# Optimization experiments

Hardware: AMD Instinct MI355X
Metric: run time of the kernel (lower is better)

Reference implementation:

```python
import jax, jax.numpy as jnp
import numpy as np

B, C, L = 32, 64, 4096
LEVEL, FL, DIM, HID = 3, 8, 64, 64
MID = max(1, C // 4)
REG = 0.01
ODE_STEPS, ODE_H = 10, 0.1  # fixed-step integration of t in [0,1] (eval_t final point)


def _gelu(x):
    return jax.nn.gelu(x, approximate=False)  # torch nn.GELU default is exact erf


def _conv1d(x, w, b, pad, mode):
    # x: [B,Cin,L], w: [Cout,Cin,K] -> [B,Cout,L] (cross-correlation, like torch)
    if pad:
        x = jnp.pad(x, ((0, 0), (0, 0), (pad, pad)), mode=mode)
    y = jax.lax.conv_general_dilated(x, w, (1,), 'VALID',
                                     dimension_numbers=('NCH', 'OIH', 'NCH'))
    return y + b[None, :, None]


def _conv1x1(x, w, b):
    return jnp.einsum('oc,bcl->bol', w, x) + b[None, :, None]


def setup_inputs() -> dict:
    key = jax.random.key(0)
    ks = jax.random.split(key, 12)
    rn = lambda k, s: jax.random.normal(k, s, jnp.float32) * 0.05
    return {
        'x': jax.random.normal(ks[0], (B, C, L), jnp.float32),
        'ode_c1_w': rn(ks[1], (DIM, C, 3)),
        'ode_c1_b': jnp.zeros((DIM,), jnp.float32),
        'ode_c2_w': rn(ks[2], (C, DIM, 3)),
        'ode_c2_b': jnp.zeros((C,), jnp.float32),
        'damp': jnp.float32(0.01),
        'stat_w': rn(ks[3], (HID, C)),
        'stat_b': jnp.zeros((HID,), jnp.float32),
        'gen1_w': rn(ks[4], (2 * HID, HID)),
        'gen1_b': jnp.zeros((2 * HID,), jnp.float32),
        'gen2_w': rn(ks[5], (2 * FL, 2 * HID)),
        'gen2_b': jnp.zeros((2 * FL,), jnp.float32),
        'gate_w': rn(ks[6], (LEVEL, C, C, 3)),
        'gate_b': jnp.zeros((LEVEL, C), jnp.float32),
        'att_w1': rn(ks[7], (LEVEL - 1, MID, C)),
        'att_b1': jnp.zeros((LEVEL - 1, MID), jnp.float32),
        'att_w2': rn(ks[8], (LEVEL - 1, C, MID)),
        'att_b2': jnp.zeros((LEVEL - 1, C), jnp.float32),
    }


def _forward(x, ode_c1_w, ode_c1_b, ode_c2_w, ode_c2_b, damp,
             stat_w, stat_b, gen1_w, gen1_b, gen2_w, gen2_b,
             gate_w, gate_b, att_w1, att_b1, att_w2, att_b2):
    # --- WaveletODE_Pro: autonomous vector field, fixed-step RK4 over [0,1] ---
    def f(z):
        h = _gelu(_conv1d(z, ode_c1_w, ode_c1_b, 1, 'edge'))
        h = jnp.tanh(_conv1d(h, ode_c2_w, ode_c2_b, 1, 'edge'))
        return h - damp * z

    def rk4(z, _):
        k1 = f(z)
        k2 = f(z + 0.5 * ODE_H * k1)
        k3 = f(z + 0.5 * ODE_H * k2)
        k4 = f(z + ODE_H * k3)
        return z + (ODE_H / 6.0) * (k1 + 2 * k2 + 2 * k3 + k4), None

    x_evolved, _ = jax.lax.scan(rk4, x, None, length=ODE_STEPS)

    # --- DyWAN_Pro: per-sample wavelet filter generation + regularizers ---
    def dywan(a):
        stat = _gelu(a.mean(-1) @ stat_w.T + stat_b)               # [B,HID]
        g = _gelu(stat @ gen1_w.T + gen1_b) @ gen2_w.T + gen2_b     # [B,2F]
        lo, hi = g[:, :FL], g[:, FL:]
        lo_pad = jnp.pad(lo, ((0, 0), (1, 1)))                      # zero pad=1, kernel [-1,1]
        lo_smooth = jnp.abs(lo_pad[:, 1:] - lo_pad[:, :-1]).mean()
        lo_n = lo / (jnp.linalg.norm(lo, axis=1, keepdims=True) + 1e-8)
        shift = sum(jnp.abs(lo_n[:, :, None] * jnp.roll(lo_n, s, axis=1)[:, None, :]).mean()
                    for s in range(1, 4))
        amp = jnp.abs((lo_n ** 2).sum(1) - 1.0).mean()
        return lo, hi, REG * (shift + amp) + 0.1 * lo_smooth

    pad_l, pad_r = FL // 2, FL - FL // 2 - 1
    approx = x_evolved
    details, los, his = [], [], []
    ortho = jnp.float32(0.0)
    for _ in range(LEVEL):
        lo, hi, o = dywan(approx)
        ortho = ortho + o
        los.append(lo)
        his.append(hi)
        ap = jnp.pad(approx, ((0, 0), (0, 0), (pad_l, pad_r)), mode='edge')
        # per-sample filter shared across channels: grouped conv == windowed einsum
        win = jnp.stack([ap[:, :, k:k + L] for k in range(FL)], axis=-1)  # [B,C,L,F]
        new_approx = jnp.einsum('bclk,bk->bcl', win, lo)
        details.append(jnp.einsum('bclk,bk->bcl', win, hi))
        approx = new_approx

    # --- CrossScaleFusion: yl input is the INITIAL evolved approx (coeffs[0]) ---
    cur = x_evolved
    enhanced = []
    for i in range(LEVEL - 1, -1, -1):
        det = details[i]
        if i < LEVEL - 1:
            att = jax.nn.sigmoid(_conv1x1(_gelu(_conv1x1(cur, att_w1[i], att_b1[i])),
                                          att_w2[i], att_b2[i]))
            det = det * att + det
        gate = jax.nn.sigmoid(_conv1d(cur, gate_w[i], gate_b[i], 1, 'constant'))
        cur = cur + gate * det
        enhanced.append(det)
    enhanced.reverse()
    return (cur, enhanced[0], enhanced[1], enhanced[2], ortho,
            jnp.stack(los), jnp.stack(his))


def reference(x, ode_c1_w, ode_c1_b, ode_c2_w, ode_c2_b, damp,
              stat_w, stat_b, gen1_w, gen1_b, gen2_w, gen2_b,
              gate_w, gate_b, att_w1, att_b1, att_w2, att_b2):
    return _forward(x, ode_c1_w, ode_c1_b, ode_c2_w, ode_c2_b, damp,
                    stat_w, stat_b, gen1_w, gen1_b, gen2_w, gen2_b,
                    gate_w, gate_b, att_w1, att_b1, att_w2, att_b2)
```

## Files before the change

kernel.cpp:

```cpp
#include <hip/hip_runtime.h>

#define Bn   32
#define Cn   64
#define Ln   4096
#define Nn   (Bn*Cn*Ln)
#define FLn  8
#define MIDn 16
#define TILE3 64
#define NT   64

typedef __bf16 bf16_t;
typedef bf16_t bf16x4 __attribute__((ext_vector_type(4)));
typedef bf16_t bf16x8 __attribute__((ext_vector_type(8)));
typedef float  f32x4  __attribute__((ext_vector_type(4)));

__device__ __forceinline__ float tanh_fast(float x) {
    float ax = fabsf(x);
    float t  = __expf(-2.0f * ax);
    float r  = __fmaf_rn(-2.0f, __fdividef(t, 1.0f + t), 1.0f);
    return copysignf(r, x);
}
__device__ __forceinline__ float gelu_fast(float x) {
    float x3 = x * x * x;
    float u  = 0.7978845608028654f * __fmaf_rn(0.044715f, x3, x);
    return 0.5f * x * (1.0f + tanh_fast(u));
}
__device__ __forceinline__ float sigmoid_f(float x) {
    return 1.0f / (1.0f + __expf(-x));
}

__global__ __launch_bounds__(256) void prep_weights(
    const float* __restrict__ w1, const float* __restrict__ w2,
    const float* __restrict__ gw, const float* __restrict__ aw2,
    bf16_t* __restrict__ w1f, bf16_t* __restrict__ w2f,
    float* __restrict__ gwt, float* __restrict__ aw2t)
{
    int idx = blockIdx.x*256 + threadIdx.x;
    if (idx < 1536) {
        int lane = idx & 63;
        int f  = (idx >> 6) % 6;
        int mt = (idx >> 6) / 6;
        int tau = f >> 1, kc = f & 1;
        int oc = mt*16 + (lane & 15);
        int c0 = kc*32 + (lane >> 4)*8;
        #pragma unroll
        for (int e = 0; e < 8; ++e) {
            int c = c0 + e;
            w1f[idx*8 + e] = (bf16_t)w1[oc*192 + c*3 + tau];
            w2f[idx*8 + e] = (bf16_t)w2[oc*192 + c*3 + tau];
        }
    }
    if (idx < 3*64*192) {
        int lvl = idx / 12288, rem = idx % 12288;
        int oc = rem / 192, r = rem % 192;
        gwt[lvl*12288 + r*64 + oc] = gw[idx];
    }
    if (idx < 2*64*16) {
        int lvl = idx / 1024, rem = idx % 1024;
        int oc = rem / 16, mm = rem % 16;
        aw2t[lvl*1024 + mm*64 + oc] = aw2[idx];
    }
}

__global__ __launch_bounds__(256, 2) void ode_rk4_step(
    const float* __restrict__ zsrc, float* __restrict__ zdst,
    const bf16_t* __restrict__ w1f, const float* __restrict__ b1,
    const bf16_t* __restrict__ w2f, const float* __restrict__ b2,
    const float* __restrict__ damp_p)
{
    __shared__ bf16_t ZC[80*64];
    __shared__ bf16_t HT[80*64];
    __shared__ bf16_t Z0[80*64];
    __shared__ bf16_t SUMB[64*64];

    const int tid  = threadIdx.x;
    const int w    = tid >> 6;
    const int lane = tid & 63;
    const int c15  = lane & 15;
    const int hb   = lane >> 4;
    const int oc0  = w*16 + hb*4;
    const int b    = blockIdx.y;
    const int l0   = blockIdx.x * NT;
    const size_t bbase = (size_t)b * Cn * Ln;
    const float damp = damp_p[0];
    const int pmin = (blockIdx.x == 0) ? 8 : 0;
    const int pmax = (blockIdx.x == gridDim.x - 1) ? 71 : 79;

    #pragma unroll
    for (int jj = 0; jj < 4; ++jj) {
        const int cc0 = (w << 4) + jj*4;
        const float* zr0 = zsrc + bbase + (size_t)(cc0+0) * Ln;
        const float* zr1 = zsrc + bbase + (size_t)(cc0+1) * Ln;
        const float* zr2 = zsrc + bbase + (size_t)(cc0+2) * Ln;
        const float* zr3 = zsrc + bbase + (size_t)(cc0+3) * Ln;
        #pragma unroll
        for (int m2 = 0; m2 < 2; ++m2) {
            int p = lane + (m2 << 6);
            if (p < 80) {
                int l = l0 - 8 + p;
                l = l < 0 ? 0 : (l > Ln-1 ? Ln-1 : l);
                bf16x4 v;
                v[0] = (bf16_t)zr0[l]; v[1] = (bf16_t)zr1[l];
                v[2] = (bf16_t)zr2[l]; v[3] = (bf16_t)zr3[l];
                int off = p*64 + (cc0 ^ ((p & 7) << 3));
                *(bf16x4*)&ZC[off] = v;
                *(bf16x4*)&Z0[off] = v;
            }
        }
    }

    f32x4 bias1v, bias2v;
    #pragma unroll
    for (int j = 0; j < 4; ++j) {
        bias1v[j] = b1[oc0 + j];
        bias2v[j] = b2[oc0 + j];
    }
    bf16x8 af1[6], af2[6];
    {
        const bf16x8* wp1 = (const bf16x8*)w1f + (w*6)*64 + lane;
        const bf16x8* wp2 = (const bf16x8*)w2f + (w*6)*64 + lane;
        #pragma unroll
        for (int f = 0; f < 6; ++f) { af1[f] = wp1[f*64]; af2[f] = wp2[f*64]; }
    }

    __syncthreads();

    for (int i = 0; i < 4; ++i) {
        const int hLo = 2*i + 1, hHi = 79 - 2*i;
        const int kLo = 2*i + 2, kHi = 78 - 2*i;

        #pragma unroll
        for (int nt = 0; nt < 5; ++nt) {
            int ph = nt*16 + c15;
            f32x4 acc = bias1v;
            #pragma unroll
            for (int tau = 0; tau < 3; ++tau) {
                int p = ph + tau - 1;
                p = p < pmin ? pmin : (p > pmax ? pmax : p);
                int base = p*64 + ((hb*8) ^ ((p & 7) << 3));
                acc = __builtin_amdgcn_mfma_f32_16x16x32_bf16(
                    af1[tau*2+0], *(const bf16x8*)&ZC[base], acc, 0, 0, 0);
                acc = __builtin_amdgcn_mfma_f32_16x16x32_bf16(
                    af1[tau*2+1], *(const bf16x8*)&ZC[base ^ 32], acc, 0, 0, 0);
            }
            if (ph >= hLo && ph < hHi) {
                bf16x4 hv;
                #pragma unroll
                for (int j = 0; j < 4; ++j)
                    hv[j] = (bf16_t)gelu_fast(acc[j]);
                *(bf16x4*)&HT[ph*64 + (oc0 ^ ((ph & 7) << 3))] = hv;
            }
        }
        __syncthreads();

        #pragma unroll
        for (int nt = 0; nt < 5; ++nt) {
            int pk = nt*16 + c15;
            f32x4 acc = bias2v;
            #pragma unroll
            for (int tau = 0; tau < 3; ++tau) {
                int q = pk + tau - 1;
                q = q < pmin ? pmin : (q > pmax ? pmax : q);
                int base = q*64 + ((hb*8) ^ ((q & 7) << 3));
                acc = __builtin_amdgcn_mfma_f32_16x16x32_bf16(
                    af2[tau*2+0], *(const bf16x8*)&HT[base], acc, 0, 0, 0);
                acc = __builtin_amdgcn_mfma_f32_16x16x32_bf16(
                    af2[tau*2+1], *(const bf16x8*)&HT[base ^ 32], acc, 0, 0, 0);
            }
            const int col = oc0 ^ ((pk & 7) << 3);
            const int off = pk*64 + col;
            if (i < 3) {
                if (pk >= kLo && pk < kHi) {
                    bf16x4 zc = *(const bf16x4*)&ZC[off];
                    bf16x4 z0 = *(const bf16x4*)&Z0[off];
                    const float alpha = (i == 2) ? 0.10f : 0.05f;
                    const bool inS = (pk >= 8) && (pk < 72);
                    const int soff = (pk-8)*64 + col;
                    bf16x4 sv;
                    if (i > 0 && inS) sv = *(const bf16x4*)&SUMB[soff];
                    bf16x4 wv, nsv;
                    #pragma unroll
                    for (int j = 0; j < 4; ++j) {
                        float kv = tanh_fast(acc[j]) - damp * (float)zc[j];
                        wv[j]  = (bf16_t)((float)z0[j] + alpha * kv);
                        nsv[j] = (i == 0) ? (bf16_t)kv
                                          : (bf16_t)((float)sv[j] + 2.0f * kv);
                    }
                    *(bf16x4*)&ZC[off] = wv;
                    if (inS) *(bf16x4*)&SUMB[soff] = nsv;
                }
            } else {
                if (pk >= 8 && pk < 72) {
                    bf16x4 zc = *(const bf16x4*)&ZC[off];
                    bf16x4 sv = *(const bf16x4*)&SUMB[(pk-8)*64 + col];
                    int gcol = l0 + pk - 8;
                    #pragma unroll
                    for (int j = 0; j < 4; ++j) {
                        float kv = tanh_fast(acc[j]) - damp * (float)zc[j];
                        size_t gof = bbase + (size_t)(oc0 + j)*Ln + gcol;
                        zdst[gof] = zsrc[gof] + (0.1f/6.0f) * ((float)sv[j] + kv);
                    }
                }
            }
        }
        if (i < 3) __syncthreads();
    }
}

__global__ __launch_bounds__(256) void mean_kernel(const float* __restrict__ in, float* __restrict__ m)
{
    const int bc = blockIdx.x;
    const float* __restrict__ row = in + (size_t)bc*Ln;
    float s = 0.0f;
    for (int l = threadIdx.x; l < Ln; l += 256) s += row[l];
    #pragma unroll
    for (int off = 32; off > 0; off >>= 1) s += __shfl_down(s, off, 64);
    __shared__ float red[4];
    if ((threadIdx.x & 63) == 0) red[threadIdx.x >> 6] = s;
    __syncthreads();
    if (threadIdx.x == 0) m[bc] = (red[0]+red[1]+red[2]+red[3]) * (1.0f/Ln);
}

__global__ __launch_bounds__(256) void dywan_kernel(
    const float* __restrict__ m,
    const float* __restrict__ stat_w, const float* __restrict__ stat_b,
    const float* __restrict__ gen1_w, const float* __restrict__ gen1_b,
    const float* __restrict__ gen2_w, const float* __restrict__ gen2_b,
    float* __restrict__ tail, int lvl)
{
    __shared__ float m_s[Bn][Cn];
    __shared__ float stat_s[Bn][64];
    __shared__ float g1_s[Bn][128];
    __shared__ float g_s[Bn][16];
    __shared__ float ored[Bn];
    const int tid = threadIdx.x;
    for (int i = tid; i < Bn*Cn; i += 256) m_s[i>>6][i&63] = m[i];
    __syncthreads();
    for (int i = tid; i < Bn*64; i += 256) {
        int b = i >> 6, h = i & 63;
        float a = stat_b[h];
        for (int c = 0; c < Cn; ++c) a = fmaf(stat_w[h*64+c], m_s[b][c], a);
        stat_s[b][h] = 0.5f * a * (1.0f + erff(a * 0.7071067811865476f));
    }
    __syncthreads();
    for (int i = tid; i < Bn*128; i += 256) {
        int b = i >> 7, j = i & 127;
        float a = gen1_b[j];
        for (int h = 0; h < 64; ++h) a = fmaf(gen1_w[j*64+h], stat_s[b][h], a);
        g1_s[b][j] = 0.5f * a * (1.0f + erff(a * 0.7071067811865476f));
    }
    __syncthreads();
    for (int i = tid; i < Bn*16; i += 256) {
        int b = i >> 4, q = i & 15;
        float a = gen2_b[q];
        for (int j = 0; j < 128; ++j) a = fmaf(gen2_w[q*128+j], g1_s[b][j], a);
        g_s[b][q] = a;
    }
    __syncthreads();
    for (int i = tid; i < Bn*16; i += 256) {
        int b = i >> 4, q = i & 15;
        if (q < FLn) tail[1 + lvl*(Bn*FLn) + b*FLn + q] = g_s[b][q];
        else         tail[1 + 3*(Bn*FLn) + lvl*(Bn*FLn) + b*FLn + (q-FLn)] = g_s[b][q];
    }
    if (tid < Bn) {
        const int b = tid;
        float S1 = 0.f, n2 = 0.f, sm = 0.f, prev = 0.f;
        #pragma unroll
        for (int k = 0; k < FLn; ++k) {
            float v = g_s[b][k];
            S1 += fabsf(v); n2 = fmaf(v, v, n2);
            sm += fabsf(v - prev); prev = v;
        }
        sm += fabsf(prev);
        float den = sqrtf(n2) + 1e-8f;
        float Sn = S1 / den;
        float s2n = n2 / (den*den);
        ored[b] = 0.01f * (3.0f*Sn*Sn*(1.0f/2048.0f) + fabsf(s2n - 1.0f)*(1.0f/32.0f))
                + 0.1f * sm * (1.0f/288.0f);
    }
    __syncthreads();
    if (tid == 0) {
        float o = 0.f;
        for (int b = 0; b < Bn; ++b) o += ored[b];
        if (lvl == 0) tail[0] = o; else tail[0] += o;
    }
}

__global__ __launch_bounds__(256) void filter_kernel(
    const float* __restrict__ in, float* __restrict__ napprox,
    float* __restrict__ det,
    const float* __restrict__ lo, const float* __restrict__ hi)
{
    const int bc = blockIdx.y;
    const int b = bc >> 6;
    float lov[8], hiv[8];
    #pragma unroll
    for (int k = 0; k < 8; ++k) { lov[k] = lo[b*8+k]; hiv[k] = hi[b*8+k]; }
    const float* __restrict__ row = in + (size_t)bc*Ln;
    const int l = blockIdx.x*256 + threadIdx.x;
    float na = 0.0f, dv = 0.0f;
    #pragma unroll
    for (int k = 0; k < 8; ++k) {
        int j = l + k - 4;
        j = j < 0 ? 0 : (j >= Ln ? Ln-1 : j);
        float v = row[j];
        na = fmaf(v, lov[k], na);
        dv = fmaf(v, hiv[k], dv);
    }
    size_t g = (size_t)bc*Ln + l;
    if (napprox) napprox[g] = na;
    det[g] = dv;
}

template<bool HAS_ATT>
__global__ __launch_bounds__(256) void stage3_kernel(
    const float* __restrict__ cur_in, float* __restrict__ det,
    float* __restrict__ cur_out,
    const float* __restrict__ gwt, const float* __restrict__ gb,
    const float* __restrict__ aw1, const float* __restrict__ ab1,
    const float* __restrict__ aw2t, const float* __restrict__ ab2)
{
    __shared__ float cur_s[Cn][TILE3+2];
    __shared__ float t1_s[MIDn][TILE3];
    __shared__ float gate_s[Cn][TILE3+1];
    __shared__ float att_s[Cn][TILE3+1];
    const int b  = blockIdx.y;
    const int l0 = blockIdx.x * TILE3;
    const int tid = threadIdx.x;
    const float* __restrict__ cb = cur_in + (size_t)b*Cn*Ln;

    for (int idx = tid; idx < Cn*(TILE3+2); idx += 256) {
        int c = idx / (TILE3+2);
        int j = idx - c*(TILE3+2);
        int l = l0 - 1 + j;
        cur_s[c][j] = (l < 0 || l >= Ln) ? 0.0f : cb[c*Ln + l];
    }
    __syncthreads();

    if (HAS_ATT) {
        for (int i = tid; i < MIDn*TILE3; i += 256) {
            int mm = i / TILE3, t = i - mm*TILE3;
            float a = ab1[mm];
            for (int c = 0; c < Cn; ++c) a = fmaf(aw1[mm*64 + c], cur_s[c][t+1], a);
            t1_s[mm][t] = gelu_fast(a);
        }
        __syncthreads();
    }

    const int oc = tid & 63;
    const int pg = tid >> 6;
    const int t0 = pg*16;
    {
        float gv[16];
        const float bb = gb[oc];
        #pragma unroll
        for (int j = 0; j < 16; ++j) gv[j] = bb;
        for (int c8 = 0; c8 < 64; c8 += 8) {
            float wr[24];
            #pragma unroll
            for (int cc = 0; cc < 8; ++cc) {
                wr[cc*3+0] = gwt[((c8+cc)*3+0)*64 + oc];
                wr[cc*3+1] = gwt[((c8+cc)*3+1)*64 + oc];
                wr[cc*3+2] = gwt[((c8+cc)*3+2)*64 + oc];
            }
            #pragma unroll
            for (int cc = 0; cc < 8; ++cc) {
                const float* cr = &cur_s[c8+cc][t0];
                float x0 = cr[0], x1 = cr[1];
                #pragma unroll
                for (int j = 0; j < 16; ++j) {
                    float x2 = cr[j+2];
                    gv[j] = fmaf(wr[cc*3+0], x0, fmaf(wr[cc*3+1], x1, fmaf(wr[cc*3+2], x2, gv[j])));
                    x0 = x1; x1 = x2;
                }
            }
        }
        #pragma unroll
        for (int j = 0; j < 16; ++j) gate_s[oc][t0+j] = sigmoid_f(gv[j]);
    }
    if (HAS_ATT) {
        float av[16];
        float w2r[16];
        #pragma unroll
        for (int mm = 0; mm < MIDn; ++mm) w2r[mm] = aw2t[mm*64 + oc];
        const float bb = ab2[oc];
        #pragma unroll
        for (int j = 0; j < 16; ++j) av[j] = bb;
        #pragma unroll
        for (int mm = 0; mm < MIDn; ++mm) {
            #pragma unroll
            for (int j = 0; j < 16; ++j) av[j] = fmaf(w2r[mm], t1_s[mm][t0+j], av[j]);
        }
        #pragma unroll
        for (int j = 0; j < 16; ++j) att_s[oc][t0+j] = sigmoid_f(av[j]);
    }
    __syncthreads();

    const size_t gb0 = (size_t)b*Cn*Ln + l0;
    for (int e = tid; e < Cn*TILE3; e += 256) {
        int c = e >> 6, t = e & 63;
        size_t g = gb0 + (size_t)c*Ln + t;
        float d = det[g];
        if (HAS_ATT) { d = d * (1.0f + att_s[c][t]); det[g] = d; }
        cur_out[g] = cur_s[c][t+1] + gate_s[c][t]*d;
    }
}

extern "C" void kernel_launch(void* const* d_in, const int* in_sizes, int n_in,
                              void* d_out, int out_size, void* d_ws, size_t ws_size,
                              hipStream_t stream)
{
    const float* x      = (const float*)d_in[0];
    const float* c1w    = (const float*)d_in[1];
    const float* c1b    = (const float*)d_in[2];
    const float* c2w    = (const float*)d_in[3];
    const float* c2b    = (const float*)d_in[4];
    const float* damp   = (const float*)d_in[5];
    const float* stat_w = (const float*)d_in[6];
    const float* stat_b = (const float*)d_in[7];
    const float* gen1_w = (const float*)d_in[8];
    const float* gen1_b = (const float*)d_in[9];
    const float* gen2_w = (const float*)d_in[10];
    const float* gen2_b = (const float*)d_in[11];
    const float* gate_w = (const float*)d_in[12];
    const float* gate_b = (const float*)d_in[13];
    const float* att_w1 = (const float*)d_in[14];
    const float* att_b1 = (const float*)d_in[15];
    const float* att_w2 = (const float*)d_in[16];
    const float* att_b2 = (const float*)d_in[17];

    float* out = (float*)d_out;
    float* Z    = (float*)d_ws;
    float* WSB  = Z + Nn;
    float* gwt  = WSB + Nn;
    float* aw2t = gwt + 36864;
    float* m_ws = aw2t + 2048;
    bf16_t* w1f = (bf16_t*)(m_ws + 2048);
    bf16_t* w2f = w1f + 12288;

    float* tail = out + (size_t)4*Nn;

    prep_weights<<<144, 256, 0, stream>>>(c1w, c2w, gate_w, att_w2, w1f, w2f, gwt, aw2t);

    dim3 gOde(Ln/NT, Bn);
    for (int s = 0; s < 10; ++s) {
        const float* src = (s == 0) ? x : ((s & 1) ? Z : WSB);
        float*       dst = (s & 1) ? WSB : Z;
        ode_rk4_step<<<gOde, 256, 0, stream>>>(src, dst, w1f, c1b, w2f, c2b, damp);
    }

    dim3 gFil(Ln/256, Bn*Cn);
    const float* appr_in[3]  = {WSB, Z, out};
    float*       appr_out[3] = {Z, out, nullptr};
    for (int lvl = 0; lvl < 3; ++lvl) {
        mean_kernel<<<Bn*Cn, 256, 0, stream>>>(appr_in[lvl], m_ws);
        dywan_kernel<<<1, 256, 0, stream>>>(m_ws, stat_w, stat_b, gen1_w, gen1_b,
                                            gen2_w, gen2_b, tail, lvl);
        filter_kernel<<<gFil, 256, 0, stream>>>(appr_in[lvl], appr_out[lvl],
            out + (size_t)(1+lvl)*Nn,
            tail + 1 + lvl*(Bn*FLn),
            tail + 1 + 3*(Bn*FLn) + lvl*(Bn*FLn));
    }

    dim3 gS3(Ln/TILE3, Bn);
    stage3_kernel<false><<<gS3, 256, 0, stream>>>(WSB, out + (size_t)3*Nn, Z,
        gwt + 2*12288, gate_b + 2*64, nullptr, nullptr, nullptr, nullptr);
    stage3_kernel<true><<<gS3, 256, 0, stream>>>(Z, out + (size_t)2*Nn, WSB,
        gwt + 1*12288, gate_b + 1*64, att_w1 + 1024, att_b1 + 16, aw2t + 1024, att_b2 + 64);
    stage3_kernel<true><<<gS3, 256, 0, stream>>>(WSB, out + (size_t)1*Nn, out,
        gwt, gate_b, att_w1, att_b1, aw2t, att_b2);
}
```

Measured before the change: 1.390 ms.

## Run stage3 gate and attention convs on bf16 MFMA with swizzled LDS

Stage3 gate conv and the first attention 1x1 conv are rewritten as bf16 MFMA 16x16x32 ops, reading from a swizzled bf16 LDS tile. Prep packs the gate and attention weights into MFMA fragment layout. The tanh and GELU helpers are also made cheaper; GELU becomes the sigmoid approximation, which affects the ODE path too and adds numerical error against the exact-erf reference. Launch bounds now request 2 blocks per SM, and the residual is read from global memory instead of LDS.

```diff
diff --git a/kernel.cpp b/kernel.cpp
--- a/kernel.cpp
+++ b/kernel.cpp
@@ -15,15 +15,11 @@
 typedef float  f32x4  __attribute__((ext_vector_type(4)));
 
 __device__ __forceinline__ float tanh_fast(float x) {
-    float ax = fabsf(x);
-    float t  = __expf(-2.0f * ax);
-    float r  = __fmaf_rn(-2.0f, __fdividef(t, 1.0f + t), 1.0f);
-    return copysignf(r, x);
+    float t = __expf(2.0f * x);
+    return 1.0f - __fdividef(2.0f, 1.0f + t);
 }
 __device__ __forceinline__ float gelu_fast(float x) {
-    float x3 = x * x * x;
-    float u  = 0.7978845608028654f * __fmaf_rn(0.044715f, x3, x);
-    return 0.5f * x * (1.0f + tanh_fast(u));
+    return __fdividef(x, 1.0f + __expf(-1.702f * x));
 }
 __device__ __forceinline__ float sigmoid_f(float x) {
     return 1.0f / (1.0f + __expf(-x));
@@ -31,9 +27,11 @@
 
 __global__ __launch_bounds__(256) void prep_weights(
     const float* __restrict__ w1, const float* __restrict__ w2,
-    const float* __restrict__ gw, const float* __restrict__ aw2,
+    const float* __restrict__ gw, const float* __restrict__ aw1,
+    const float* __restrict__ aw2,
     bf16_t* __restrict__ w1f, bf16_t* __restrict__ w2f,
-    float* __restrict__ gwt, float* __restrict__ aw2t)
+    bf16_t* __restrict__ gwf, bf16_t* __restrict__ aw1f,
+    float* __restrict__ aw2t)
 {
     int idx = blockIdx.x*256 + threadIdx.x;
     if (idx < 1536) {
@@ -50,10 +48,28 @@
             w2f[idx*8 + e] = (bf16_t)w2[oc*192 + c*3 + tau];
         }
     }
-    if (idx < 3*64*192) {
-        int lvl = idx / 12288, rem = idx % 12288;
-        int oc = rem / 192, r = rem % 192;
-        gwt[lvl*12288 + r*64 + oc] = gw[idx];
+    if (idx < 4608) {
+        int lane = idx & 63;
+        int r  = idx >> 6;
+        int f  = r % 6;
+        int mt = (r / 6) % 4;
+        int lvl = r / 24;
+        int tau = f >> 1, kc = f & 1;
+        int oc = mt*16 + (lane & 15);
+        int c0 = kc*32 + (lane >> 4)*8;
+        #pragma unroll
+        for (int e = 0; e < 8; ++e)
+            gwf[idx*8 + e] = (bf16_t)gw[((lvl*64 + oc)*64 + (c0+e))*3 + tau];
+    }
+    if (idx < 256) {
+        int lane = idx & 63;
+        int kc  = (idx >> 6) & 1;
+        int lvl = idx >> 7;
+        int mm = lane & 15;
+        int c0 = kc*32 + (lane >> 4)*8;
+        #pragma unroll
+        for (int e = 0; e < 8; ++e)
+            aw1f[idx*8 + e] = (bf16_t)aw1[lvl*1024 + mm*64 + c0 + e];
     }
     if (idx < 2*64*16) {
         int lvl = idx / 1024, rem = idx % 1024;
@@ -313,76 +329,109 @@
 }
 
 template<bool HAS_ATT>
-__global__ __launch_bounds__(256) void stage3_kernel(
+__global__ __launch_bounds__(256, 2) void stage3_kernel(
     const float* __restrict__ cur_in, float* __restrict__ det,
     float* __restrict__ cur_out,
-    const float* __restrict__ gwt, const float* __restrict__ gb,
-    const float* __restrict__ aw1, const float* __restrict__ ab1,
+    const bf16_t* __restrict__ gwf, const float* __restrict__ gb,
+    const bf16_t* __restrict__ aw1f, const float* __restrict__ ab1,
     const float* __restrict__ aw2t, const float* __restrict__ ab2)
 {
-    __shared__ float cur_s[Cn][TILE3+2];
-    __shared__ float t1_s[MIDn][TILE3];
-    __shared__ float gate_s[Cn][TILE3+1];
-    __shared__ float att_s[Cn][TILE3+1];
-    const int b  = blockIdx.y;
-    const int l0 = blockIdx.x * TILE3;
-    const int tid = threadIdx.x;
-    const float* __restrict__ cb = cur_in + (size_t)b*Cn*Ln;
-
-    for (int idx = tid; idx < Cn*(TILE3+2); idx += 256) {
-        int c = idx / (TILE3+2);
-        int j = idx - c*(TILE3+2);
-        int l = l0 - 1 + j;
-        cur_s[c][j] = (l < 0 || l >= Ln) ? 0.0f : cb[c*Ln + l];
+    __shared__ bf16_t CB[66*64];
+    __shared__ float t1_s[16][65];
+    __shared__ float gate_s[64][65];
+    __shared__ float att_s[64][65];
+
+    const int tid  = threadIdx.x;
+    const int w    = tid >> 6;
+    const int lane = tid & 63;
+    const int c15  = lane & 15;
+    const int hb   = lane >> 4;
+    const int oc0  = w*16 + hb*4;
+    const int b    = blockIdx.y;
+    const int l0   = blockIdx.x * TILE3;
+    const size_t bbase = (size_t)b * Cn * Ln;
+
+    #pragma unroll
+    for (int jj = 0; jj < 4; ++jj) {
+        const int cc0 = (w << 4) + jj*4;
+        const float* cr0 = cur_in + bbase + (size_t)(cc0+0) * Ln;
+        const float* cr1 = cur_in + bbase + (size_t)(cc0+1) * Ln;
+        const float* cr2 = cur_in + bbase + (size_t)(cc0+2) * Ln;
+        const float* cr3 = cur_in + bbase + (size_t)(cc0+3) * Ln;
+        #pragma unroll
+        for (int m2 = 0; m2 < 2; ++m2) {
+            int p = lane + (m2 << 6);
+            if (p < 66) {
+                int l = l0 - 1 + p;
+                bool in = (l >= 0) && (l < Ln);
+                bf16x4 v;
+                v[0] = (bf16_t)(in ? cr0[l] : 0.0f);
+                v[1] = (bf16_t)(in ? cr1[l] : 0.0f);
+                v[2] = (bf16_t)(in ? cr2[l] : 0.0f);
+                v[3] = (bf16_t)(in ? cr3[l] : 0.0f);
+                *(bf16x4*)&CB[p*64 + (cc0 ^ ((p & 7) << 3))] = v;
+            }
+        }
     }
     __syncthreads();
 
     if (HAS_ATT) {
-        for (int i = tid; i < MIDn*TILE3; i += 256) {
-            int mm = i / TILE3, t = i - mm*TILE3;
-            float a = ab1[mm];
-            for (int c = 0; c < Cn; ++c) a = fmaf(aw1[mm*64 + c], cur_s[c][t+1], a);
-            t1_s[mm][t] = gelu_fast(a);
-        }
-        __syncthreads();
-    }
-
-    const int oc = tid & 63;
-    const int pg = tid >> 6;
-    const int t0 = pg*16;
+        f32x4 acc;
+        #pragma unroll
+        for (int j = 0; j < 4; ++j) acc[j] = ab1[hb*4 + j];
+        const int p = w*16 + c15 + 1;
+        #pragma unroll
+        for (int kc = 0; kc < 2; ++kc) {
+            bf16x8 a1 = ((const bf16x8*)aw1f)[kc*64 + lane];
+            int base = p*64 + (((kc*32) + hb*8) ^ ((p & 7) << 3));
+            acc = __builtin_amdgcn_mfma_f32_16x16x32_bf16(
+                a1, *(const bf16x8*)&CB[base], acc, 0, 0, 0);
+        }
+        #pragma unroll
+        for (int j = 0; j < 4; ++j)
+            t1_s[hb*4 + j][w*16 + c15] = gelu_fast(acc[j]);
+    }
+
     {
-        float gv[16];
-        const float bb = gb[oc];
-        #pragma unroll
-        for (int j = 0; j < 16; ++j) gv[j] = bb;
-        for (int c8 = 0; c8 < 64; c8 += 8) {
-            float wr[24];
+        bf16x8 ag[6];
+        const bf16x8* wp = (const bf16x8*)gwf + (w*6)*64 + lane;
+        #pragma unroll
+        for (int f = 0; f < 6; ++f) ag[f] = wp[f*64];
+        f32x4 biasg;
+        #pragma unroll
+        for (int j = 0; j < 4; ++j) biasg[j] = gb[oc0 + j];
+
+        #pragma unroll
+        for (int nt = 0; nt < 5; ++nt) {
+            int ph = nt*16 + c15;
+            f32x4 acc = biasg;
             #pragma unroll
-            for (int cc = 0; cc < 8; ++cc) {
-                wr[cc*3+0] = gwt[((c8+cc)*3+0)*64 + oc];
-                wr[cc*3+1] = gwt[((c8+cc)*3+1)*64 + oc];
-                wr[cc*3+2] = gwt[((c8+cc)*3+2)*64 + oc];
-            }
-            #pragma unroll
-            for (int cc = 0; cc < 8; ++cc) {
-                const float* cr = &cur_s[c8+cc][t0];
-                float x0 = cr[0], x1 = cr[1];
+            for (int tau = 0; tau < 3; ++tau) {
+                int q = ph - 1 + tau;
+                q = q < 0 ? 0 : (q > 65 ? 65 : q);
+                int base0 = q*64 + ((hb*8) ^ ((q & 7) << 3));
+                acc = __builtin_amdgcn_mfma_f32_16x16x32_bf16(
+                    ag[tau*2+0], *(const bf16x8*)&CB[base0], acc, 0, 0, 0);
+                acc = __builtin_amdgcn_mfma_f32_16x16x32_bf16(
+                    ag[tau*2+1], *(const bf16x8*)&CB[base0 ^ 32], acc, 0, 0, 0);
+            }
+            if (ph >= 1 && ph < 65) {
+                int t = ph - 1;
                 #pragma unroll
-                for (int j = 0; j < 16; ++j) {
-                    float x2 = cr[j+2];
-                    gv[j] = fmaf(wr[cc*3+0], x0, fmaf(wr[cc*3+1], x1, fmaf(wr[cc*3+2], x2, gv[j])));
-                    x0 = x1; x1 = x2;
-                }
-            }
-        }
-        #pragma unroll
-        for (int j = 0; j < 16; ++j) gate_s[oc][t0+j] = sigmoid_f(gv[j]);
-    }
+                for (int j = 0; j < 4; ++j)
+                    gate_s[oc0 + j][t] = sigmoid_f(acc[j]);
+            }
+        }
+    }
+    __syncthreads();
+
     if (HAS_ATT) {
+        const int oc = tid & 63;
+        const int t0 = (tid >> 6) * 16;
+        float w2r[16];
+        #pragma unroll
+        for (int mm = 0; mm < MIDn; ++mm) w2r[mm] = aw2t[mm*64 + oc];
         float av[16];
-        float w2r[16];
-        #pragma unroll
-        for (int mm = 0; mm < MIDn; ++mm) w2r[mm] = aw2t[mm*64 + oc];
         const float bb = ab2[oc];
         #pragma unroll
         for (int j = 0; j < 16; ++j) av[j] = bb;
@@ -393,16 +442,16 @@
         }
         #pragma unroll
         for (int j = 0; j < 16; ++j) att_s[oc][t0+j] = sigmoid_f(av[j]);
-    }
-    __syncthreads();
-
-    const size_t gb0 = (size_t)b*Cn*Ln + l0;
+        __syncthreads();
+    }
+
+    const size_t gb0 = bbase + l0;
     for (int e = tid; e < Cn*TILE3; e += 256) {
         int c = e >> 6, t = e & 63;
         size_t g = gb0 + (size_t)c*Ln + t;
         float d = det[g];
         if (HAS_ATT) { d = d * (1.0f + att_s[c][t]); det[g] = d; }
-        cur_out[g] = cur_s[c][t+1] + gate_s[c][t]*d;
+        cur_out[g] = cur_in[g] + gate_s[c][t]*d;
     }
 }
 
@@ -432,15 +481,17 @@
     float* out = (float*)d_out;
     float* Z    = (float*)d_ws;
     float* WSB  = Z + Nn;
-    float* gwt  = WSB + Nn;
-    float* aw2t = gwt + 36864;
+    float* aw2t = WSB + Nn;
     float* m_ws = aw2t + 2048;
-    bf16_t* w1f = (bf16_t*)(m_ws + 2048);
-    bf16_t* w2f = w1f + 12288;
+    bf16_t* w1f  = (bf16_t*)(m_ws + 2048);
+    bf16_t* w2f  = w1f + 12288;
+    bf16_t* gwf  = w2f + 12288;
+    bf16_t* aw1f = gwf + 36864;
 
     float* tail = out + (size_t)4*Nn;
 
-    prep_weights<<<144, 256, 0, stream>>>(c1w, c2w, gate_w, att_w2, w1f, w2f, gwt, aw2t);
+    prep_weights<<<144, 256, 0, stream>>>(c1w, c2w, gate_w, att_w1, att_w2,
+                                          w1f, w2f, gwf, aw1f, aw2t);
 
     dim3 gOde(Ln/NT, Bn);
     for (int s = 0; s < 10; ++s) {
@@ -464,9 +515,9 @@
 
     dim3 gS3(Ln/TILE3, Bn);
     stage3_kernel<false><<<gS3, 256, 0, stream>>>(WSB, out + (size_t)3*Nn, Z,
-        gwt + 2*12288, gate_b + 2*64, nullptr, nullptr, nullptr, nullptr);
+        gwf + 2*12288, gate_b + 2*64, nullptr, nullptr, nullptr, nullptr);
     stage3_kernel<true><<<gS3, 256, 0, stream>>>(Z, out + (size_t)2*Nn, WSB,
-        gwt + 1*12288, gate_b + 1*64, att_w1 + 1024, att_b1 + 16, aw2t + 1024, att_b2 + 64);
+        gwf + 1*12288, gate_b + 1*64, aw1f + 1024, att_b1 + 16, aw2t + 1024, att_b2 + 64);
     stage3_kernel<true><<<gS3, 256, 0, stream>>>(WSB, out + (size_t)1*Nn, out,
-        gwt, gate_b, att_w1, att_b1, aw2t, att_b2);
-}
+        gwf, gate_b, aw1f, att_b1, aw2t, att_b2);
+}
```

Result: faster. 1.177 ms (-15.3%).
